# Kernel optimization log

Measured on AMD Instinct MI355X. Metric: run time of the kernel, lower is better.

## Reference

```python
import jax, jax.numpy as jnp
import numpy as np

H, W, K = 256, 256, 3          # three 256x256 operand label matrices (last is target)
N = K * H * W                  # total labels / logits per sample
LANE = 8                       # memory_lane_width
NROWS = N // LANE              # memory grid rows (N divisible by 8)
NOPS = H * W                   # one STORE op per target cell


def _staged(h, exp):
    # staged cache-penalty: base = h**exp scaled by cache-level factor
    base = jnp.power(h, exp)
    f = jnp.where(h <= 2.0, 1.0,
        jnp.where(h <= 4.0, 1.5,
        jnp.where(h <= 8.0, 2.0,
        jnp.where(h <= 16.0, 3.0, 5.0))))
    return jnp.sum(base * f, axis=-1)


def setup_inputs() -> dict:
    key = jax.random.key(0)
    ks = jax.random.split(key, 7)
    B = 8
    return {
        "mem_logits_batch": jax.random.normal(ks[0], (B, N), jnp.float32),
        "conv1_w": jax.random.normal(ks[1], (K * 8, 1, 3, 3), jnp.float32) * 0.02,
        "conv1_b": jax.random.normal(ks[2], (K * 8,), jnp.float32) * 0.02,
        "conv2_w": jax.random.normal(ks[3], (16, 8, 3, 3), jnp.float32) * 0.02,
        "conv2_b": jax.random.normal(ks[4], (16,), jnp.float32) * 0.02,
        "proj_w": jax.random.normal(ks[5], (NOPS, 16 * 4 * 4), jnp.float32) * 0.02,
        "proj_b": jax.random.normal(ks[6], (NOPS,), jnp.float32) * 0.02,
    }


def reference(mem_logits_batch, conv1_w, conv1_b, conv2_w, conv2_b, proj_w, proj_b):
    B = mem_logits_batch.shape[0]
    dn = ("NCHW", "OIHW", "NCHW")

    # addr_map: label i (labels are all distinct, contiguous per matrix) -> argsort(logits)[i]
    addr = jnp.argsort(mem_logits_batch, axis=-1)              # [B, N] permutation of 0..N-1

    # per-matrix address images; grouped conv = K independent 1->8 convs
    x = addr.astype(jnp.float32).reshape(B, K, H, W)           # [B, K, H, W]
    feat = jax.lax.conv_general_dilated(x, conv1_w, (1, 1), "SAME",
                                        dimension_numbers=dn, feature_group_count=K)
    feat = jax.nn.relu(feat + conv1_b[None, :, None, None])    # [B, K*8, H, W]

    # scatter feat columns into memory grid at their addresses.
    # addr is a full permutation -> scatter == gather with inverse permutation.
    feats_flat = feat.reshape(B, K, 8, H * W).transpose(0, 2, 1, 3).reshape(B, 8, N)
    inv = jnp.argsort(addr, axis=-1)                           # [B, N]
    mem = jnp.take_along_axis(feats_flat, inv[:, None, :], axis=2)
    mem = mem.reshape(B, 8, NROWS, LANE)                       # [B, 8, NROWS, 8]

    mem2 = jax.lax.conv_general_dilated(mem, conv2_w, (1, 1), "SAME", dimension_numbers=dn)
    mem2 = jax.nn.relu(mem2 + conv2_b[None, :, None, None])    # [B, 16, NROWS, 8]

    # AdaptiveAvgPool2d((4,4)): dims divisible -> uniform block mean
    pooled = mem2.reshape(B, 16, 4, NROWS // 4, 4, LANE // 4).mean(axis=(3, 5))  # [B,16,4,4]
    flat = pooled.reshape(B, 16 * 4 * 4)
    op_logits = flat @ proj_w.T + proj_b                       # [B, NOPS]

    # order operations by op logits; op t reads addr[k*HW+t] for sources, dst = last matrix
    perm = jnp.argsort(op_logits, axis=-1)                     # [B, NOPS]
    S = addr.reshape(B, K, NOPS).transpose(0, 2, 1)            # [B, NOPS, K] = [src0, src1, dst]
    S_ord = jnp.take_along_axis(S, perm[:, :, None], axis=1).astype(jnp.float32)

    # intra-op hops: along each op's [src..., dst] sequence
    intra_d = (S_ord[:, :, 1:] - S_ord[:, :, :-1]).reshape(B, -1)   # [B, NOPS*(K-1)]
    # inter-op hops: first addr of op minus dst addr of previous op
    inter_d = S_ord[:, 1:, 0] - S_ord[:, :-1, -1]                   # [B, NOPS-1]

    intra_pen = _staged(jax.nn.relu(intra_d), 1.0) + _staged(jax.nn.relu(-intra_d), 2.0)
    inter_pen = _staged(jax.nn.relu(inter_d), 1.0) + _staged(jax.nn.relu(-inter_d), 2.0)
    return inter_pen, intra_pen
```

## Files before the change

### kernel.cpp

```cpp
#include <hip/hip_runtime.h>
#include <stdint.h>

typedef unsigned int u32;
typedef unsigned long long u64;

#define BN 8
#define HW_ 65536
#define N1 196608
#define NOPS_ 65536
#define NROWS_ 24576
#define NB1 192
#define NB2 64

__device__ __forceinline__ u32 fkey(float x) {
  u32 u = __float_as_uint(x);
  return u ^ ((u & 0x80000000u) ? 0xFFFFFFFFu : 0x80000000u);
}

template <bool FIRST>
__global__ __launch_bounds__(256) void rs_hist(const u64* __restrict__ kv, const float* __restrict__ xf,
                                               u32* __restrict__ hist, u32* __restrict__ gTot,
                                               int n, int nblk, int shift) {
  __shared__ u32 h[256];
  int t = threadIdx.x;
  int b = blockIdx.x / nblk, blk = blockIdx.x % nblk;
  h[t] = 0;
  __syncthreads();
  if (FIRST) {
    const float* xp = xf + (size_t)b * n + (size_t)blk * 1024;
#pragma unroll
    for (int j = 0; j < 4; ++j) {
      u32 d = fkey(xp[j * 256 + t]) & 255u;
      atomicAdd(&h[d], 1u);
    }
  } else {
    const u64* kp = kv + (size_t)b * n + (size_t)blk * 1024;
#pragma unroll
    for (int j = 0; j < 4; ++j) {
      u32 d = (u32)(kp[j * 256 + t] >> (32 + shift)) & 255u;
      atomicAdd(&h[d], 1u);
    }
  }
  __syncthreads();
  hist[((size_t)b * 256 + t) * nblk + blk] = h[t];
  atomicAdd(&gTot[b * 256 + t], h[t]);
}

__device__ __forceinline__ u32 wscan_incl(u32 x, int lane) {
#pragma unroll
  for (int off = 1; off < 64; off <<= 1) {
    u32 y = __shfl_up(x, off, 64);
    if (lane >= off) x += y;
  }
  return x;
}

__global__ __launch_bounds__(256) void rs_scanB(u32* __restrict__ hist, const u32* __restrict__ gTot, int nblk) {
  int t = threadIdx.x, w = t >> 6, lane = t & 63;
  int b = blockIdx.x >> 6, dgrp = blockIdx.x & 63;
  int d = dgrp * 4 + w;
  const u32* gt = gTot + b * 256;
  u32 base = 0, run = 0;
  int dc = d >> 6, dl = d & 63;
#pragma unroll
  for (int c = 0; c < 4; ++c) {
    u32 v = gt[c * 64 + lane];
    u32 incl = wscan_incl(v, lane);
    if (c == dc) base = run + __shfl(incl - v, dl, 64);
    run += __shfl(incl, 63, 64);
  }
  u32* p = hist + ((size_t)b * 256 + d) * nblk;
  u32 acc = base;
  for (int c = 0; c < nblk; c += 64) {
    u32 v = p[c + lane];
    u32 incl = wscan_incl(v, lane);
    p[c + lane] = acc + incl - v;
    acc += __shfl(incl, 63, 64);
  }
}

template <bool FIRST, bool FINAL>
__global__ __launch_bounds__(256) void rs_scatter(const u64* __restrict__ kvIn, const float* __restrict__ xf,
                                                  u64* __restrict__ out64, u32* __restrict__ out32,
                                                  const u32* __restrict__ hist, int n, int nblk, int shift) {
  __shared__ u32 sBase[256];
  __shared__ u32 cnt[16][256];
  __shared__ u32 dpre[256];
  __shared__ u32 wsum[4];
  __shared__ u64 stage[1024];
  int t = threadIdx.x, lane = t & 63, wid = t >> 6;
  int b = blockIdx.x / nblk, blk = blockIdx.x % nblk;
  u64 kvr[4]; u32 dg[4];
  if (FIRST) {
    const float* xp = xf + (size_t)b * n + (size_t)blk * 1024;
#pragma unroll
    for (int j = 0; j < 4; ++j) {
      u32 k = fkey(xp[j * 256 + t]);
      kvr[j] = ((u64)k << 32) | (u32)(blk * 1024 + j * 256 + t);
      dg[j] = k & 255u;
    }
  } else {
    const u64* kp = kvIn + (size_t)b * n + (size_t)blk * 1024;
#pragma unroll
    for (int j = 0; j < 4; ++j) {
      kvr[j] = kp[j * 256 + t];
      dg[j] = (u32)(kvr[j] >> (32 + shift)) & 255u;
    }
  }
  sBase[t] = hist[((size_t)b * 256 + t) * nblk + blk];
#pragma unroll
  for (int r = 0; r < 16; ++r) cnt[r][t] = 0;
  __syncthreads();
  u64 lmask = (1ull << lane) - 1ull;
  u32 rw[4];
#pragma unroll
  for (int j = 0; j < 4; ++j) {
    u32 d = dg[j];
    u64 peers = ~0ull;
#pragma unroll
    for (int bit = 0; bit < 8; ++bit) {
      u64 bal = __ballot((d >> bit) & 1);
      peers &= ((d >> bit) & 1) ? bal : ~bal;
    }
    u64 lower = peers & lmask;
    rw[j] = (u32)__popcll(lower);
    if (lower == 0) cnt[j * 4 + wid][d] = (u32)__popcll(peers);
  }
  __syncthreads();
  u32 run = 0;
#pragma unroll
  for (int r = 0; r < 16; ++r) { u32 c = cnt[r][t]; cnt[r][t] = run; run += c; }
  u32 incl = wscan_incl(run, lane);
  if (lane == 63) wsum[wid] = incl;
  __syncthreads();
  u32 woff = 0;
#pragma unroll
  for (int w = 0; w < 4; ++w) if (w < wid) woff += wsum[w];
  dpre[t] = woff + incl - run;
  __syncthreads();
#pragma unroll
  for (int j = 0; j < 4; ++j) {
    u32 d = dg[j];
    u32 lpos = dpre[d] + cnt[j * 4 + wid][d] + rw[j];
    stage[lpos] = kvr[j];
  }
  __syncthreads();
#pragma unroll
  for (int s = 0; s < 4; ++s) {
    int i = s * 256 + t;
    u64 kv = stage[i];
    u32 d = (u32)(kv >> (32 + shift)) & 255u;
    u32 g = sBase[d] + ((u32)i - dpre[d]);
    if (FINAL) out32[(size_t)b * n + g] = (u32)kv;
    else out64[(size_t)b * n + g] = kv;
  }
}

__global__ __launch_bounds__(256) void conv1_scatter(const u32* __restrict__ addr, const float* __restrict__ w1,
                                                     const float* __restrict__ b1, float* __restrict__ mem,
                                                     uint4* __restrict__ addr3) {
  __shared__ float ax[34][34];
  __shared__ float ws[8][9];
  __shared__ float bs[8];
  int t = threadIdx.x;
  int blk = blockIdx.x;
  int tile = blk & 63; int bk2 = blk >> 6; int k = bk2 % 3; int b = bk2 / 3;
  int ty = tile >> 3, tx = tile & 7;
  if (t < 72) ws[t / 9][t % 9] = w1[k * 72 + t];
  if (t >= 128 && t < 136) bs[t - 128] = b1[k * 8 + (t - 128)];
  const u32* ap = addr + (size_t)b * N1 + (size_t)k * HW_;
  for (int idx = t; idx < 34 * 34; idx += 256) {
    int y = idx / 34, x = idx % 34;
    int h = ty * 32 + y - 1, w = tx * 32 + x - 1;
    float v = 0.f;
    if (h >= 0 && h < 256 && w >= 0 && w < 256) v = (float)ap[h * 256 + w];
    ax[y][x] = v;
  }
  __syncthreads();
  float* mb = mem + (size_t)b * N1 * 8;
  const u32* adb = addr + (size_t)b * N1;
  uint4* a3b = addr3 + (size_t)b * HW_;
#pragma unroll
  for (int s = 0; s < 4; ++s) {
    int p = t + s * 256;
    int y = p >> 5, x = p & 31;
    float f[8];
#pragma unroll
    for (int c = 0; c < 8; ++c) f[c] = bs[c];
#pragma unroll
    for (int dy = 0; dy < 3; ++dy)
#pragma unroll
      for (int dx = 0; dx < 3; ++dx) {
        float v = ax[y + dy][x + dx];
#pragma unroll
        for (int c = 0; c < 8; ++c) f[c] = fmaf(ws[c][dy * 3 + dx], v, f[c]);
      }
    u32 a = (u32)ax[y + 1][x + 1];
    float4* dst = reinterpret_cast<float4*>(mb + (size_t)a * 8);
    float4 lo = make_float4(fmaxf(f[0], 0.f), fmaxf(f[1], 0.f), fmaxf(f[2], 0.f), fmaxf(f[3], 0.f));
    float4 hi = make_float4(fmaxf(f[4], 0.f), fmaxf(f[5], 0.f), fmaxf(f[6], 0.f), fmaxf(f[7], 0.f));
    dst[0] = lo; dst[1] = hi;
    if (k == 0) {
      int gp = (ty * 32 + y) * 256 + tx * 32 + x;
      a3b[gp] = make_uint4(a, adb[HW_ + gp], adb[2 * HW_ + gp], 0u);
    }
  }
}

__global__ __launch_bounds__(256, 3) void c2p1(const float* __restrict__ mem, const float* __restrict__ w2,
                                               const float* __restrict__ b2, float* __restrict__ gPartial) {
  __shared__ float tile[98 * 68];
  __shared__ float w2s[1152];
  __shared__ float b2s[16];
  __shared__ float red[16][64];
  int blk = blockIdx.x; int sub = blk & 255; int b = blk >> 8;
  int r0 = sub * 96;
  int t = threadIdx.x;
  for (int idx = t; idx < 1152; idx += 256) w2s[idx] = w2[idx];
  if (t < 16) b2s[t] = b2[t];
  const float* mb = mem + (size_t)b * (N1 * 8);
  for (int q = t; q < 98 * 16; q += 256) {
    int ti = q >> 4, qw = q & 15;
    int r = r0 - 1 + ti;
    float4 v = make_float4(0.f, 0.f, 0.f, 0.f);
    if (r >= 0 && r < NROWS_) v = *reinterpret_cast<const float4*>(mb + (size_t)r * 64 + qw * 4);
    *reinterpret_cast<float4*>(&tile[ti * 68 + qw * 4]) = v;
  }
  __syncthreads();
  int co = t & 15, rowgrp = t >> 4;
  float wreg[3][3][8];
#pragma unroll
  for (int ci = 0; ci < 8; ++ci)
#pragma unroll
    for (int kr = 0; kr < 3; ++kr)
#pragma unroll
      for (int kc = 0; kc < 3; ++kc)
        wreg[kr][kc][ci] = w2s[(co * 8 + ci) * 9 + kr * 3 + kc];
  float bias = b2s[co];
  float pool[4] = {0.f, 0.f, 0.f, 0.f};
#define CSTEP(V, CI) do { \
    if (j < 3) { \
      if (li >= 1) s0[li - 1] = fmaf((V), wreg[j][2][CI], s0[li - 1]); \
      s0[li] = fmaf((V), wreg[j][1][CI], s0[li]); \
      if (li < 7) s0[li + 1] = fmaf((V), wreg[j][0][CI], s0[li + 1]); \
    } \
    if (j >= 1) { \
      if (li >= 1) s1[li - 1] = fmaf((V), wreg[j - 1][2][CI], s1[li - 1]); \
      s1[li] = fmaf((V), wreg[j - 1][1][CI], s1[li]); \
      if (li < 7) s1[li + 1] = fmaf((V), wreg[j - 1][0][CI], s1[li + 1]); \
    } \
  } while (0)
#pragma unroll 1
  for (int i = 0; i < 3; ++i) {
    int lr0 = rowgrp * 2 + 32 * i;
    float s0[8], s1[8];
#pragma unroll
    for (int l = 0; l < 8; ++l) { s0[l] = 0.f; s1[l] = 0.f; }
#pragma unroll
    for (int j = 0; j < 4; ++j) {
      const float* trow = &tile[(lr0 + j) * 68];
#pragma unroll
      for (int li = 0; li < 8; ++li) {
        float4 aa = *reinterpret_cast<const float4*>(trow + li * 8);
        float4 bb = *reinterpret_cast<const float4*>(trow + li * 8 + 4);
        CSTEP(aa.x, 0); CSTEP(aa.y, 1); CSTEP(aa.z, 2); CSTEP(aa.w, 3);
        CSTEP(bb.x, 4); CSTEP(bb.y, 5); CSTEP(bb.z, 6); CSTEP(bb.w, 7);
      }
    }
#pragma unroll
    for (int l = 0; l < 8; ++l)
      pool[l >> 1] += fmaxf(s0[l] + bias, 0.f) + fmaxf(s1[l] + bias, 0.f);
  }
#undef CSTEP
#pragma unroll
  for (int lb = 0; lb < 4; ++lb) red[rowgrp][lb * 16 + co] = pool[lb];
  __syncthreads();
  if (t < 64) {
    float s = 0.f;
#pragma unroll
    for (int rg = 0; rg < 16; ++rg) s += red[rg][t];
    int rb = sub >> 6, subW = sub & 63;
    gPartial[(((size_t)(b * 4 + rb) * 64 + subW) * 64) + t] = s;
  }
}

__global__ void c2p2(const float* __restrict__ gPartial, float* __restrict__ flatS) {
  int b = blockIdx.x; int t = threadIdx.x;
  int ch = t >> 4; int rb = (t >> 2) & 3; int lb = t & 3;
  float s = 0.f;
  for (int sub = 0; sub < 64; ++sub)
    s += gPartial[(((size_t)(b * 4 + rb) * 64 + sub) * 64) + lb * 16 + ch];
  flatS[b * 256 + t] = s * (1.0f / 12288.0f);
}

__global__ __launch_bounds__(256) void proj_k(const float* __restrict__ flatS, const float* __restrict__ pw,
                                              const float* __restrict__ pb, u64* __restrict__ kv2) {
  __shared__ float fs[8][256];
  int t = threadIdx.x;
  for (int i = t; i < 2048; i += 256) fs[i >> 8][i & 255] = flatS[i];
  __syncthreads();
  int q = t & 15; int og = t >> 4;
  int o = blockIdx.x * 16 + og;
  float acc[8];
#pragma unroll
  for (int b = 0; b < 8; ++b) acc[b] = 0.f;
  const float* wr = pw + (size_t)o * 256;
#pragma unroll
  for (int j = 0; j < 16; ++j) {
    float w = wr[q + 16 * j];
#pragma unroll
    for (int b = 0; b < 8; ++b) acc[b] = fmaf(fs[b][q + 16 * j], w, acc[b]);
  }
#pragma unroll
  for (int m = 1; m < 16; m <<= 1)
#pragma unroll
    for (int b = 0; b < 8; ++b) acc[b] += __shfl_xor(acc[b], m, 64);
  if (q == 0) {
    float bias = pb[o];
#pragma unroll
    for (int b = 0; b < 8; ++b) {
      u32 k = fkey(acc[b] + bias);
      kv2[(size_t)b * NOPS_ + o] = ((u64)k << 32) | (u32)o;
    }
  }
}

__device__ __forceinline__ double stagedp(float d) {
  double h, base;
  if (d >= 0.f) { h = (double)d; base = h; }
  else { h = (double)(-d); base = h * h; }
  double f = (h <= 2.0) ? 1.0 : (h <= 4.0) ? 1.5 : (h <= 8.0) ? 2.0 : (h <= 16.0) ? 3.0 : 5.0;
  return base * f;
}

__global__ __launch_bounds__(256) void penalty_k(const u32* __restrict__ perm, const uint4* __restrict__ addr3,
                                                 double* __restrict__ partials, u32* __restrict__ ctr,
                                                 float* __restrict__ out) {
  int b = blockIdx.x >> 6; int blk = blockIdx.x & 63;
  int t = threadIdx.x, lane = t & 63;
  const u32* pm = perm + (size_t)b * NOPS_;
  const uint4* a3 = addr3 + (size_t)b * HW_;
  double intra = 0.0, inter = 0.0;
#pragma unroll
  for (int s = 0; s < 4; ++s) {
    int tg = blk * 1024 + s * 256 + t;
    u32 p = pm[tg];
    uint4 g = a3[p];
    float a0 = (float)g.x, a1 = (float)g.y, a2 = (float)g.z;
    intra += stagedp(a1 - a0) + stagedp(a2 - a1);
    float a2p = __shfl_up(a2, 1, 64);
    if (lane == 0 && tg > 0) {
      u32 pp = pm[tg - 1];
      a2p = (float)a3[pp].z;
    }
    if (tg > 0) inter += stagedp(a0 - a2p);
  }
#pragma unroll
  for (int m = 1; m < 64; m <<= 1) {
    intra += __shfl_xor(intra, m, 64);
    inter += __shfl_xor(inter, m, 64);
  }
  __shared__ double red[4][2];
  __shared__ u32 lastFlag;
  int wid = t >> 6;
  if (lane == 0) { red[wid][0] = inter; red[wid][1] = intra; }
  __syncthreads();
  if (t == 0) {
    double i0 = red[0][0] + red[1][0] + red[2][0] + red[3][0];
    double i1 = red[0][1] + red[1][1] + red[2][1] + red[3][1];
    partials[((size_t)b * 64 + blk) * 2 + 0] = i0;
    partials[((size_t)b * 64 + blk) * 2 + 1] = i1;
    __threadfence();
    u32 done = atomicAdd(ctr, 1u);
    lastFlag = (done == (u32)(BN * 64 - 1));
  }
  __syncthreads();
  if (lastFlag) {
    __threadfence();
    if (t < 16) {
      int which = t >> 3, bb = t & 7;
      double s = 0.0;
      for (int k = 0; k < 64; ++k) s += partials[((size_t)bb * 64 + k) * 2 + which];
      out[which * 8 + bb] = (float)s;
    }
  }
}

extern "C" void kernel_launch(void* const* d_in, const int* in_sizes, int n_in,
                              void* d_out, int out_size, void* d_ws, size_t ws_size,
                              hipStream_t stream) {
  const float* logits = (const float*)d_in[0];
  const float* w1 = (const float*)d_in[1];
  const float* b1 = (const float*)d_in[2];
  const float* w2 = (const float*)d_in[3];
  const float* b2 = (const float*)d_in[4];
  const float* pw = (const float*)d_in[5];
  const float* pb = (const float*)d_in[6];
  float* out = (float*)d_out;

  char* ws = (char*)d_ws;
  size_t o = 0;
  auto take = [&](size_t bytes) { char* p = ws + o; o += (bytes + 255) & ~(size_t)255; return p; };
  u64* kv1A = (u64*)take((size_t)BN * N1 * 8);
  u64* kv1B = (u64*)take((size_t)BN * N1 * 8);
  u64* kv2A = (u64*)take((size_t)BN * NOPS_ * 8);
  u64* kv2B = (u64*)take((size_t)BN * NOPS_ * 8);
  u32* hist = (u32*)take((size_t)256 * NB1 * BN * 4);
  u32* gTotAll = (u32*)take(((size_t)8 * BN * 256 + 64) * 4);
  u32* addr = (u32*)take((size_t)BN * N1 * 4);
  float* mem = (float*)take((size_t)BN * N1 * 8 * 4);
  float* gPartial = (float*)take((size_t)BN * 4 * 64 * 64 * 4);
  float* flatS = (float*)take((size_t)BN * 256 * 4);
  u32* perm = (u32*)take((size_t)BN * NOPS_ * 4);
  double* partials = (double*)take((size_t)BN * 64 * 2 * 8);
  uint4* addr3 = (uint4*)kv1A;
  u32* ctr = gTotAll + (size_t)8 * BN * 256;

  hipMemsetAsync(gTotAll, 0, ((size_t)8 * BN * 256 + 64) * 4, stream);

  {
    u32* gT = gTotAll;
    rs_hist<true><<<BN * NB1, 256, 0, stream>>>(nullptr, logits, hist, gT, N1, NB1, 0);
    rs_scanB<<<BN * 64, 256, 0, stream>>>(hist, gT, NB1);
    rs_scatter<true, false><<<BN * NB1, 256, 0, stream>>>(nullptr, logits, kv1B, nullptr, hist, N1, NB1, 0);
  }
  u64* src = kv1B; u64* dst = kv1A;
  for (int p = 1; p < 4; ++p) {
    u32* gT = gTotAll + (size_t)p * BN * 256;
    rs_hist<false><<<BN * NB1, 256, 0, stream>>>(src, nullptr, hist, gT, N1, NB1, p * 8);
    rs_scanB<<<BN * 64, 256, 0, stream>>>(hist, gT, NB1);
    if (p < 3) {
      rs_scatter<false, false><<<BN * NB1, 256, 0, stream>>>(src, nullptr, dst, nullptr, hist, N1, NB1, p * 8);
      u64* tmp = src; src = dst; dst = tmp;
    } else {
      rs_scatter<false, true><<<BN * NB1, 256, 0, stream>>>(src, nullptr, nullptr, addr, hist, N1, NB1, p * 8);
    }
  }

  conv1_scatter<<<BN * 3 * 64, 256, 0, stream>>>(addr, w1, b1, mem, addr3);

  c2p1<<<BN * 256, 256, 0, stream>>>(mem, w2, b2, gPartial);
  c2p2<<<BN, 256, 0, stream>>>(gPartial, flatS);

  proj_k<<<NOPS_ / 16, 256, 0, stream>>>(flatS, pw, pb, kv2A);

  src = kv2A; dst = kv2B;
  for (int p = 0; p < 4; ++p) {
    u32* gT = gTotAll + (size_t)(4 + p) * BN * 256;
    rs_hist<false><<<BN * NB2, 256, 0, stream>>>(src, nullptr, hist, gT, NOPS_, NB2, p * 8);
    rs_scanB<<<BN * 64, 256, 0, stream>>>(hist, gT, NB2);
    if (p < 3) {
      rs_scatter<false, false><<<BN * NB2, 256, 0, stream>>>(src, nullptr, dst, nullptr, hist, NOPS_, NB2, p * 8);
      u64* tmp = src; src = dst; dst = tmp;
    } else {
      rs_scatter<false, true><<<BN * NB2, 256, 0, stream>>>(src, nullptr, nullptr, perm, hist, NOPS_, NB2, p * 8);
    }
  }

  penalty_k<<<BN * 64, 256, 0, stream>>>(perm, addr3, partials, ctr, out);
}
```

Measured before the change: 291.3 us.

## Replace per-pass hist/scan/scatter radix sort with onesweep decoupled look-back

Both radix sorts move from three kernels per digit pass (per-block histogram, scan, scatter) to one upfront histogram kernel that counts all four digits at once, a tiny global-offset scan, and one single-pass scatter kernel per digit. That kernel finds each tile's prefix through decoupled look-back over flagged per-tile counts, using an atomic tile counter to keep tile order. This removes two kernel launches and a full key re-read per pass, as well as the large per-block histogram arrays. In exchange it adds spin-waiting on earlier tiles and depends on forward-progress ordering. The look-back buffer for the first sort reuses the mem buffer.

New measurement: 375.0 us. +28.7%, slower.

```diff
diff --git a/kernel.cpp b/kernel.cpp
--- a/kernel.cpp
+++ b/kernel.cpp
@@ -11,41 +11,13 @@
 #define NROWS_ 24576
 #define NB1 192
 #define NB2 64
+#define LBW 32
 
 __device__ __forceinline__ u32 fkey(float x) {
   u32 u = __float_as_uint(x);
   return u ^ ((u & 0x80000000u) ? 0xFFFFFFFFu : 0x80000000u);
 }
 
-template <bool FIRST>
-__global__ __launch_bounds__(256) void rs_hist(const u64* __restrict__ kv, const float* __restrict__ xf,
-                                               u32* __restrict__ hist, u32* __restrict__ gTot,
-                                               int n, int nblk, int shift) {
-  __shared__ u32 h[256];
-  int t = threadIdx.x;
-  int b = blockIdx.x / nblk, blk = blockIdx.x % nblk;
-  h[t] = 0;
-  __syncthreads();
-  if (FIRST) {
-    const float* xp = xf + (size_t)b * n + (size_t)blk * 1024;
-#pragma unroll
-    for (int j = 0; j < 4; ++j) {
-      u32 d = fkey(xp[j * 256 + t]) & 255u;
-      atomicAdd(&h[d], 1u);
-    }
-  } else {
-    const u64* kp = kv + (size_t)b * n + (size_t)blk * 1024;
-#pragma unroll
-    for (int j = 0; j < 4; ++j) {
-      u32 d = (u32)(kp[j * 256 + t] >> (32 + shift)) & 255u;
-      atomicAdd(&h[d], 1u);
-    }
-  }
-  __syncthreads();
-  hist[((size_t)b * 256 + t) * nblk + blk] = h[t];
-  atomicAdd(&gTot[b * 256 + t], h[t]);
-}
-
 __device__ __forceinline__ u32 wscan_incl(u32 x, int lane) {
 #pragma unroll
   for (int off = 1; off < 64; off <<= 1) {
@@ -55,62 +27,103 @@
   return x;
 }
 
-__global__ __launch_bounds__(256) void rs_scanB(u32* __restrict__ hist, const u32* __restrict__ gTot, int nblk) {
-  int t = threadIdx.x, w = t >> 6, lane = t & 63;
-  int b = blockIdx.x >> 6, dgrp = blockIdx.x & 63;
-  int d = dgrp * 4 + w;
-  const u32* gt = gTot + b * 256;
-  u32 base = 0, run = 0;
-  int dc = d >> 6, dl = d & 63;
+__global__ __launch_bounds__(256) void histAll1(const float* __restrict__ xf, u32* __restrict__ gTot) {
+  __shared__ u32 h[4][256];
+  int t = threadIdx.x;
+  int b = blockIdx.x / 96, chunk = blockIdx.x % 96;
+#pragma unroll
+  for (int p = 0; p < 4; ++p) h[p][t] = 0;
+  __syncthreads();
+  const float* xp = xf + (size_t)b * N1 + (size_t)chunk * 2048;
+#pragma unroll
+  for (int j = 0; j < 8; ++j) {
+    u32 k = fkey(xp[j * 256 + t]);
+    atomicAdd(&h[0][k & 255u], 1u);
+    atomicAdd(&h[1][(k >> 8) & 255u], 1u);
+    atomicAdd(&h[2][(k >> 16) & 255u], 1u);
+    atomicAdd(&h[3][k >> 24], 1u);
+  }
+  __syncthreads();
+#pragma unroll
+  for (int p = 0; p < 4; ++p) {
+    u32 v = h[p][t];
+    if (v) atomicAdd(&gTot[((size_t)p * BN + b) * 256 + t], v);
+  }
+}
+
+__global__ __launch_bounds__(256) void histAll2(const u64* __restrict__ kv, u32* __restrict__ gTot) {
+  __shared__ u32 h[4][256];
+  int t = threadIdx.x;
+  int b = blockIdx.x / 64, chunk = blockIdx.x % 64;
+#pragma unroll
+  for (int p = 0; p < 4; ++p) h[p][t] = 0;
+  __syncthreads();
+  const u64* kp = kv + (size_t)b * NOPS_ + (size_t)chunk * 1024;
+#pragma unroll
+  for (int j = 0; j < 4; ++j) {
+    u32 k = (u32)(kp[j * 256 + t] >> 32);
+    atomicAdd(&h[0][k & 255u], 1u);
+    atomicAdd(&h[1][(k >> 8) & 255u], 1u);
+    atomicAdd(&h[2][(k >> 16) & 255u], 1u);
+    atomicAdd(&h[3][k >> 24], 1u);
+  }
+  __syncthreads();
+#pragma unroll
+  for (int p = 0; p < 4; ++p) {
+    u32 v = h[p][t];
+    if (v) atomicAdd(&gTot[((size_t)p * BN + b) * 256 + t], v);
+  }
+}
+
+__global__ void scanTot(const u32* __restrict__ gTot, u32* __restrict__ dBase) {
+  int v = blockIdx.x, t = threadIdx.x;
+  const u32* gt = gTot + (size_t)v * 256;
+  u32* db = dBase + (size_t)v * 256;
+  u32 run = 0;
 #pragma unroll
   for (int c = 0; c < 4; ++c) {
-    u32 v = gt[c * 64 + lane];
-    u32 incl = wscan_incl(v, lane);
-    if (c == dc) base = run + __shfl(incl - v, dl, 64);
+    u32 x = gt[c * 64 + t];
+    u32 incl = wscan_incl(x, t);
+    db[c * 64 + t] = run + incl - x;
     run += __shfl(incl, 63, 64);
   }
-  u32* p = hist + ((size_t)b * 256 + d) * nblk;
-  u32 acc = base;
-  for (int c = 0; c < nblk; c += 64) {
-    u32 v = p[c + lane];
-    u32 incl = wscan_incl(v, lane);
-    p[c + lane] = acc + incl - v;
-    acc += __shfl(incl, 63, 64);
-  }
 }
 
 template <bool FIRST, bool FINAL>
-__global__ __launch_bounds__(256) void rs_scatter(const u64* __restrict__ kvIn, const float* __restrict__ xf,
-                                                  u64* __restrict__ out64, u32* __restrict__ out32,
-                                                  const u32* __restrict__ hist, int n, int nblk, int shift) {
+__global__ __launch_bounds__(256) void rs_sweep(const u64* __restrict__ kvIn, const float* __restrict__ xf,
+                                                u64* __restrict__ out64, u32* __restrict__ out32,
+                                                const u32* __restrict__ dBase, u32* __restrict__ lb,
+                                                u32* __restrict__ tileCtr, int n, int nblk, int shift) {
   __shared__ u32 sBase[256];
   __shared__ u32 cnt[16][256];
   __shared__ u32 dpre[256];
   __shared__ u32 wsum[4];
   __shared__ u64 stage[1024];
+  __shared__ u32 tileSh;
   int t = threadIdx.x, lane = t & 63, wid = t >> 6;
-  int b = blockIdx.x / nblk, blk = blockIdx.x % nblk;
+  if (t == 0) tileSh = atomicAdd(tileCtr, 1u);
+#pragma unroll
+  for (int r = 0; r < 16; ++r) cnt[r][t] = 0;
+  __syncthreads();
+  u32 gt = tileSh;
+  int b = gt / nblk, tile = gt % nblk;
   u64 kvr[4]; u32 dg[4];
   if (FIRST) {
-    const float* xp = xf + (size_t)b * n + (size_t)blk * 1024;
+    const float* xp = xf + (size_t)b * n + (size_t)tile * 1024;
 #pragma unroll
     for (int j = 0; j < 4; ++j) {
       u32 k = fkey(xp[j * 256 + t]);
-      kvr[j] = ((u64)k << 32) | (u32)(blk * 1024 + j * 256 + t);
+      kvr[j] = ((u64)k << 32) | (u32)(tile * 1024 + j * 256 + t);
       dg[j] = k & 255u;
     }
   } else {
-    const u64* kp = kvIn + (size_t)b * n + (size_t)blk * 1024;
+    const u64* kp = kvIn + (size_t)b * n + (size_t)tile * 1024;
 #pragma unroll
     for (int j = 0; j < 4; ++j) {
       kvr[j] = kp[j * 256 + t];
       dg[j] = (u32)(kvr[j] >> (32 + shift)) & 255u;
     }
   }
-  sBase[t] = hist[((size_t)b * 256 + t) * nblk + blk];
-#pragma unroll
-  for (int r = 0; r < 16; ++r) cnt[r][t] = 0;
-  __syncthreads();
   u64 lmask = (1ull << lane) - 1ull;
   u32 rw[4];
 #pragma unroll
@@ -127,6 +140,43 @@
     if (lower == 0) cnt[j * 4 + wid][d] = (u32)__popcll(peers);
   }
   __syncthreads();
+  u32 tcnt = 0;
+#pragma unroll
+  for (int r = 0; r < 16; ++r) tcnt += cnt[r][t];
+  u32* lbRow = lb + ((size_t)b * nblk + tile) * 256;
+  if (tile > 0)
+    __hip_atomic_store(&lbRow[t], (1u << 30) | tcnt, __ATOMIC_RELAXED, __HIP_MEMORY_SCOPE_AGENT);
+  u32 acc = 0;
+  {
+    const u32* lbp = lb + (size_t)b * nblk * 256;
+    int j = tile - 1;
+    bool done = (tile == 0);
+    while (!done) {
+      u32 vals[LBW];
+#pragma unroll
+      for (int q = 0; q < LBW; ++q) {
+        int jj = j - q;
+        vals[q] = (jj >= 0)
+            ? __hip_atomic_load(&lbp[(size_t)jj * 256 + t], __ATOMIC_RELAXED, __HIP_MEMORY_SCOPE_AGENT)
+            : (2u << 30);
+      }
+      int adv = 0;
+#pragma unroll
+      for (int q = 0; q < LBW; ++q) {
+        if (adv == q && !done) {
+          u32 st = vals[q] >> 30;
+          if (st != 0u) {
+            acc += vals[q] & 0x3FFFFFFFu;
+            ++adv;
+            if (st == 2u) done = true;
+          }
+        }
+      }
+      j -= adv;
+    }
+  }
+  __hip_atomic_store(&lbRow[t], (2u << 30) | (acc + tcnt), __ATOMIC_RELAXED, __HIP_MEMORY_SCOPE_AGENT);
+  sBase[t] = dBase[b * 256 + t] + acc;
   u32 run = 0;
 #pragma unroll
   for (int r = 0; r < 16; ++r) { u32 c = cnt[r][t]; cnt[r][t] = run; run += c; }
@@ -141,8 +191,7 @@
 #pragma unroll
   for (int j = 0; j < 4; ++j) {
     u32 d = dg[j];
-    u32 lpos = dpre[d] + cnt[j * 4 + wid][d] + rw[j];
-    stage[lpos] = kvr[j];
+    stage[dpre[d] + cnt[j * 4 + wid][d] + rw[j]] = kvr[j];
   }
   __syncthreads();
 #pragma unroll
@@ -405,37 +454,33 @@
   u64* kv1B = (u64*)take((size_t)BN * N1 * 8);
   u64* kv2A = (u64*)take((size_t)BN * NOPS_ * 8);
   u64* kv2B = (u64*)take((size_t)BN * NOPS_ * 8);
-  u32* hist = (u32*)take((size_t)256 * NB1 * BN * 4);
-  u32* gTotAll = (u32*)take(((size_t)8 * BN * 256 + 64) * 4);
   u32* addr = (u32*)take((size_t)BN * N1 * 4);
   float* mem = (float*)take((size_t)BN * N1 * 8 * 4);
   float* gPartial = (float*)take((size_t)BN * 4 * 64 * 64 * 4);
   float* flatS = (float*)take((size_t)BN * 256 * 4);
   u32* perm = (u32*)take((size_t)BN * NOPS_ * 4);
   double* partials = (double*)take((size_t)BN * 64 * 2 * 8);
+  u32* lb2 = (u32*)take((size_t)4 * BN * NB2 * 256 * 4);
+  u32* gTotA = (u32*)take((size_t)2 * 4 * BN * 256 * 4);
+  u32* dBaseA = (u32*)take((size_t)2 * 4 * BN * 256 * 4);
+  u32* ctrs = (u32*)take(64 * 4);
   uint4* addr3 = (uint4*)kv1A;
-  u32* ctr = gTotAll + (size_t)8 * BN * 256;
-
-  hipMemsetAsync(gTotAll, 0, ((size_t)8 * BN * 256 + 64) * 4, stream);
-
-  {
-    u32* gT = gTotAll;
-    rs_hist<true><<<BN * NB1, 256, 0, stream>>>(nullptr, logits, hist, gT, N1, NB1, 0);
-    rs_scanB<<<BN * 64, 256, 0, stream>>>(hist, gT, NB1);
-    rs_scatter<true, false><<<BN * NB1, 256, 0, stream>>>(nullptr, logits, kv1B, nullptr, hist, N1, NB1, 0);
-  }
-  u64* src = kv1B; u64* dst = kv1A;
-  for (int p = 1; p < 4; ++p) {
-    u32* gT = gTotAll + (size_t)p * BN * 256;
-    rs_hist<false><<<BN * NB1, 256, 0, stream>>>(src, nullptr, hist, gT, N1, NB1, p * 8);
-    rs_scanB<<<BN * 64, 256, 0, stream>>>(hist, gT, NB1);
-    if (p < 3) {
-      rs_scatter<false, false><<<BN * NB1, 256, 0, stream>>>(src, nullptr, dst, nullptr, hist, N1, NB1, p * 8);
-      u64* tmp = src; src = dst; dst = tmp;
-    } else {
-      rs_scatter<false, true><<<BN * NB1, 256, 0, stream>>>(src, nullptr, nullptr, addr, hist, N1, NB1, p * 8);
-    }
-  }
+  u32* lb1 = (u32*)mem;
+
+  const size_t LB1_BYTES = (size_t)4 * BN * NB1 * 256 * 4;
+  hipMemsetAsync(lb1, 0, LB1_BYTES, stream);
+  hipMemsetAsync(lb2, 0, ((size_t)4 * BN * NB2 * 256 + 2 * 4 * BN * 256 * 2 + 64) * 4, stream);
+
+  histAll1<<<BN * 96, 256, 0, stream>>>(logits, gTotA);
+  scanTot<<<32, 64, 0, stream>>>(gTotA, dBaseA);
+  rs_sweep<true, false><<<BN * NB1, 256, 0, stream>>>(nullptr, logits, kv1B, nullptr,
+      dBaseA + 0 * BN * 256, lb1 + (size_t)0 * BN * NB1 * 256, ctrs + 0, N1, NB1, 0);
+  rs_sweep<false, false><<<BN * NB1, 256, 0, stream>>>(kv1B, nullptr, kv1A, nullptr,
+      dBaseA + 1 * BN * 256, lb1 + (size_t)1 * BN * NB1 * 256, ctrs + 1, N1, NB1, 8);
+  rs_sweep<false, false><<<BN * NB1, 256, 0, stream>>>(kv1A, nullptr, kv1B, nullptr,
+      dBaseA + 2 * BN * 256, lb1 + (size_t)2 * BN * NB1 * 256, ctrs + 2, N1, NB1, 16);
+  rs_sweep<false, true><<<BN * NB1, 256, 0, stream>>>(kv1B, nullptr, nullptr, addr,
+      dBaseA + 3 * BN * 256, lb1 + (size_t)3 * BN * NB1 * 256, ctrs + 3, N1, NB1, 24);
 
   conv1_scatter<<<BN * 3 * 64, 256, 0, stream>>>(addr, w1, b1, mem, addr3);
 
@@ -444,18 +489,16 @@
 
   proj_k<<<NOPS_ / 16, 256, 0, stream>>>(flatS, pw, pb, kv2A);
 
-  src = kv2A; dst = kv2B;
-  for (int p = 0; p < 4; ++p) {
-    u32* gT = gTotAll + (size_t)(4 + p) * BN * 256;
-    rs_hist<false><<<BN * NB2, 256, 0, stream>>>(src, nullptr, hist, gT, NOPS_, NB2, p * 8);
-    rs_scanB<<<BN * 64, 256, 0, stream>>>(hist, gT, NB2);
-    if (p < 3) {
-      rs_scatter<false, false><<<BN * NB2, 256, 0, stream>>>(src, nullptr, dst, nullptr, hist, NOPS_, NB2, p * 8);
-      u64* tmp = src; src = dst; dst = tmp;
-    } else {
-      rs_scatter<false, true><<<BN * NB2, 256, 0, stream>>>(src, nullptr, nullptr, perm, hist, NOPS_, NB2, p * 8);
-    }
-  }
-
-  penalty_k<<<BN * 64, 256, 0, stream>>>(perm, addr3, partials, ctr, out);
-}
+  histAll2<<<BN * NB2, 256, 0, stream>>>(kv2A, gTotA + 4 * BN * 256);
+  scanTot<<<32, 64, 0, stream>>>(gTotA + 4 * BN * 256, dBaseA + 4 * BN * 256);
+  rs_sweep<false, false><<<BN * NB2, 256, 0, stream>>>(kv2A, nullptr, kv2B, nullptr,
+      dBaseA + 4 * BN * 256, lb2 + (size_t)0 * BN * NB2 * 256, ctrs + 4, NOPS_, NB2, 0);
+  rs_sweep<false, false><<<BN * NB2, 256, 0, stream>>>(kv2B, nullptr, kv2A, nullptr,
+      dBaseA + 5 * BN * 256, lb2 + (size_t)1 * BN * NB2 * 256, ctrs + 5, NOPS_, NB2, 8);
+  rs_sweep<false, false><<<BN * NB2, 256, 0, stream>>>(kv2A, nullptr, kv2B, nullptr,
+      dBaseA + 6 * BN * 256, lb2 + (size_t)2 * BN * NB2 * 256, ctrs + 6, NOPS_, NB2, 16);
+  rs_sweep<false, true><<<BN * NB2, 256, 0, stream>>>(kv2B, nullptr, nullptr, perm,
+      dBaseA + 7 * BN * 256, lb2 + (size_t)3 * BN * NB2 * 256, ctrs + 7, NOPS_, NB2, 24);
+
+  penalty_k<<<BN * 64, 256, 0, stream>>>(perm, addr3, partials, ctrs + 8, out);
+}
```
